# Kernel optimization log

Measured on AMD Instinct MI355X. Metric: run time of the kernel, lower is better.

Reference implementation:

```python
import jax, jax.numpy as jnp
import numpy as np

BITS = 8
BOUND = 2 ** (BITS - 1) - 1  # 127, symmetric int8 as in AQT IntNumerics


def setup_inputs() -> dict:
    key = jax.random.key(0)
    k1, k2 = jax.random.split(key)
    lhs = jax.random.normal(k1, (8192, 4096), dtype=jnp.float32)
    rhs = jax.random.normal(k2, (4096, 4096), dtype=jnp.float32)
    return {"lhs": lhs, "rhs": rhs}


def reference(lhs, rhs):
    # Per-channel symmetric scales over the contracting dim (AQT calibration:
    # abs-max / bound). lhs contracts axis 1, rhs contracts axis 0, per
    # dimension_numbers (((1,),(0,)),((),())).
    lhs_scale = jnp.max(jnp.abs(lhs), axis=1, keepdims=True) / BOUND  # [M,1]
    rhs_scale = jnp.max(jnp.abs(rhs), axis=0, keepdims=True) / BOUND  # [1,N]
    lhs_scale = jnp.where(lhs_scale == 0, jnp.ones_like(lhs_scale), lhs_scale)
    rhs_scale = jnp.where(rhs_scale == 0, jnp.ones_like(rhs_scale), rhs_scale)

    # Quantize: round-to-nearest, clip to [-127, 127], store as int8.
    qlhs = jnp.clip(jnp.round(lhs / lhs_scale), -BOUND, BOUND).astype(jnp.int8)
    qrhs = jnp.clip(jnp.round(rhs / rhs_scale), -BOUND, BOUND).astype(jnp.int8)

    # Integer matmul with int32 accumulation (the AQT quantized dot_general).
    acc = jax.lax.dot_general(
        qlhs, qrhs,
        dimension_numbers=(((1,), (0,)), ((), ())),
        preferred_element_type=jnp.int32,
    )  # [M, N] int32

    # Inline dequant by transposed scales (scale_t): [M,1] * [1,N].
    return acc.astype(jnp.float32) * lhs_scale * rhs_scale
```

## Files before the change

### kernel.cpp

```cpp
#include <hip/hip_runtime.h>
#include <stdint.h>

#define M_DIM 8192
#define N_DIM 4096
#define K_DIM 4096

typedef int v4i __attribute__((ext_vector_type(4)));

typedef __attribute__((address_space(1))) const void gas_void;
typedef __attribute__((address_space(3))) void las_void;

__device__ __forceinline__ void async_copy16(const uint8_t* g, uint8_t* l) {
    __builtin_amdgcn_global_load_lds((gas_void*)g, (las_void*)l, 16, 0, 0);
}

__device__ __forceinline__ int quant1(float x, float scale) {
    float q = __builtin_rintf(x / scale);
    q = fminf(127.0f, fmaxf(-127.0f, q));
    return (int)q;
}

__device__ __forceinline__ uint32_t pack4(int q0, int q1, int q2, int q3) {
    return (uint32_t)(q0 & 255) | ((uint32_t)(q1 & 255) << 8) |
           ((uint32_t)(q2 & 255) << 16) | ((uint32_t)(q3 & 255) << 24);
}

__global__ __launch_bounds__(256) void quant_lhs_kernel(
    const float* __restrict__ lhs, uint8_t* __restrict__ qlhs,
    float* __restrict__ lhs_scale) {
    const int row = blockIdx.x;
    const int tid = threadIdx.x;
    const float4* src = (const float4*)(lhs + (size_t)row * K_DIM);

    float4 v[4];
    float m = 0.0f;
#pragma unroll
    for (int i = 0; i < 4; ++i) {
        v[i] = src[tid + i * 256];
        m = fmaxf(m, fmaxf(fmaxf(fabsf(v[i].x), fabsf(v[i].y)),
                           fmaxf(fabsf(v[i].z), fabsf(v[i].w))));
    }
#pragma unroll
    for (int off = 32; off > 0; off >>= 1)
        m = fmaxf(m, __shfl_down(m, off, 64));

    __shared__ float wmax[4];
    if ((tid & 63) == 0) wmax[tid >> 6] = m;
    __syncthreads();
    const float mm = fmaxf(fmaxf(wmax[0], wmax[1]), fmaxf(wmax[2], wmax[3]));
    const float scale = (mm == 0.0f) ? 1.0f : mm / 127.0f;
    if (tid == 0) lhs_scale[row] = scale;

    uint32_t* dst = (uint32_t*)(qlhs + (size_t)row * K_DIM);
#pragma unroll
    for (int i = 0; i < 4; ++i) {
        dst[tid + i * 256] = pack4(quant1(v[i].x, scale), quant1(v[i].y, scale),
                                   quant1(v[i].z, scale), quant1(v[i].w, scale));
    }
}

__global__ __launch_bounds__(256) void rhs_max_kernel(
    const float* __restrict__ rhs, uint32_t* __restrict__ maxbits) {
    const int c = blockIdx.x * 256 + threadIdx.x;
    const int r0 = blockIdx.y * 128;
    float m = 0.0f;
    for (int r = 0; r < 128; ++r)
        m = fmaxf(m, fabsf(rhs[(size_t)(r0 + r) * N_DIM + c]));
    atomicMax(&maxbits[c], __float_as_uint(m));
}

__global__ __launch_bounds__(256) void rhs_scale_kernel(
    const uint32_t* __restrict__ maxbits, float* __restrict__ rhs_scale) {
    const int c = blockIdx.x * 256 + threadIdx.x;
    const float m = __uint_as_float(maxbits[c]);
    rhs_scale[c] = (m == 0.0f) ? 1.0f : m / 127.0f;
}

__global__ __launch_bounds__(256) void quant_rhs_t_kernel(
    const float* __restrict__ rhs, const float* __restrict__ rhs_scale,
    uint8_t* __restrict__ qrhsT) {
    const int n = blockIdx.x * 256 + threadIdx.x;
    const float scale = rhs_scale[n];
    const int kbase = blockIdx.y * 256;

    for (int c16 = 0; c16 < 16; ++c16) {
        const int k0 = kbase + c16 * 16;
        uint32_t p[4];
#pragma unroll
        for (int g = 0; g < 4; ++g) {
            int q[4];
#pragma unroll
            for (int j = 0; j < 4; ++j) {
                const float x = rhs[(size_t)(k0 + g * 4 + j) * N_DIM + n];
                q[j] = quant1(x, scale);
            }
            p[g] = pack4(q[0], q[1], q[2], q[3]);
        }
        uint4 u;
        u.x = p[0]; u.y = p[1]; u.z = p[2]; u.w = p[3];
        *(uint4*)(qrhsT + (size_t)n * K_DIM + k0) = u;
    }
}

__global__ __launch_bounds__(256) void gemm_i8_kernel(
    const uint8_t* __restrict__ qlhs, const uint8_t* __restrict__ qrhsT,
    const float* __restrict__ lhs_scale, const float* __restrict__ rhs_scale,
    float* __restrict__ out) {
    __shared__ __align__(16) uint8_t As[128 * 64];
    __shared__ __align__(16) uint8_t Bs[128 * 64];

    const int tid = threadIdx.x;
    const int wave = tid >> 6;
    const int lane = tid & 63;

    const int bm = blockIdx.y * 128;
    const int bn = blockIdx.x * 128;

    const int srow = wave * 32 + (lane >> 2);
    const int scol = (lane & 3) * 16;
    const uint8_t* ga = qlhs + (size_t)(bm + srow) * K_DIM + scol;
    const uint8_t* gb = qrhsT + (size_t)(bn + srow) * K_DIM + scol;
    uint8_t* la = As + wave * 2048 + lane * 16;
    uint8_t* lb = Bs + wave * 2048 + lane * 16;
    const size_t rowstep16 = (size_t)16 * K_DIM;

    const int wm = (wave >> 1) * 64;
    const int wn = (wave & 1) * 64;
    const int fra = (wm + (lane & 15)) * 64 + (lane >> 4) * 16;
    const int frb = (wn + (lane & 15)) * 64 + (lane >> 4) * 16;

    v4i acc[4][4] = {};

    for (int k0 = 0; k0 < K_DIM; k0 += 64) {
        async_copy16(ga, la);
        async_copy16(ga + rowstep16, la + 1024);
        async_copy16(gb, lb);
        async_copy16(gb + rowstep16, lb + 1024);
        ga += 64;
        gb += 64;
        __syncthreads();

        v4i a[4], b[4];
#pragma unroll
        for (int i = 0; i < 4; ++i) a[i] = *(const v4i*)(As + fra + i * 1024);
#pragma unroll
        for (int i = 0; i < 4; ++i) b[i] = *(const v4i*)(Bs + frb + i * 1024);
#pragma unroll
        for (int mi = 0; mi < 4; ++mi)
#pragma unroll
            for (int ni = 0; ni < 4; ++ni)
                acc[mi][ni] = __builtin_amdgcn_mfma_i32_16x16x64_i8(
                    a[mi], b[ni], acc[mi][ni], 0, 0, 0);
        __syncthreads();
    }

    const int r0 = bm + wm + (lane >> 4) * 4;
    const int c0 = bn + wn + (lane & 15);
#pragma unroll
    for (int mi = 0; mi < 4; ++mi) {
        float ls[4];
#pragma unroll
        for (int r = 0; r < 4; ++r) ls[r] = lhs_scale[r0 + mi * 16 + r];
#pragma unroll
        for (int ni = 0; ni < 4; ++ni) {
            const int col = c0 + ni * 16;
            const float rs = rhs_scale[col];
            float* o = out + (size_t)(r0 + mi * 16) * N_DIM + col;
#pragma unroll
            for (int r = 0; r < 4; ++r)
                o[(size_t)r * N_DIM] = (float)acc[mi][ni][r] * ls[r] * rs;
        }
    }
}

extern "C" void kernel_launch(void* const* d_in, const int* in_sizes, int n_in,
                              void* d_out, int out_size, void* d_ws,
                              size_t ws_size, hipStream_t stream) {
    const float* lhs = (const float*)d_in[0];
    const float* rhs = (const float*)d_in[1];
    float* out = (float*)d_out;

    uint8_t* ws = (uint8_t*)d_ws;
    uint8_t* qlhs = ws;
    uint8_t* qrhsT = ws + 33554432u;
    float* lhs_scale = (float*)(ws + 50331648u);
    float* rhs_scale = (float*)(ws + 50364416u);
    uint32_t* maxbits = (uint32_t*)(ws + 50380800u);

    hipMemsetAsync(maxbits, 0, N_DIM * sizeof(uint32_t), stream);

    quant_lhs_kernel<<<M_DIM, 256, 0, stream>>>(lhs, qlhs, lhs_scale);
    rhs_max_kernel<<<dim3(N_DIM / 256, 32), 256, 0, stream>>>(rhs, maxbits);
    rhs_scale_kernel<<<N_DIM / 256, 256, 0, stream>>>(maxbits, rhs_scale);
    quant_rhs_t_kernel<<<dim3(N_DIM / 256, K_DIM / 256), 256, 0, stream>>>(
        rhs, rhs_scale, qrhsT);
    gemm_i8_kernel<<<dim3(N_DIM / 128, M_DIM / 128), 256, 0, stream>>>(
        qlhs, qrhsT, lhs_scale, rhs_scale, out);
}
```

Measured before the change: 496.9 us.

## Swizzle GEMM LDS layout, tile rhs quant-transpose through LDS, split rhs max

The int8 GEMM now XOR-swizzles the 16-byte chunk column, both when staging global data into LDS and when reading MFMA fragments, to avoid LDS bank conflicts on the fragment loads. The rhs quantize-transpose kernel is rewritten to read float4 rows coalesced, transpose 64x128 tiles through padded shared memory, and write 16-byte chunks of the transposed int8 output. Previously each thread made strided single-float loads and scattered 16-byte writes. The rhs column-max kernel uses 4x more blocks with shorter unrolled loops for more parallelism, at the cost of more atomics.

```diff
diff --git a/kernel.cpp b/kernel.cpp
--- a/kernel.cpp
+++ b/kernel.cpp
@@ -62,9 +62,10 @@
 __global__ __launch_bounds__(256) void rhs_max_kernel(
     const float* __restrict__ rhs, uint32_t* __restrict__ maxbits) {
     const int c = blockIdx.x * 256 + threadIdx.x;
-    const int r0 = blockIdx.y * 128;
+    const int r0 = blockIdx.y * 32;
     float m = 0.0f;
-    for (int r = 0; r < 128; ++r)
+#pragma unroll
+    for (int r = 0; r < 32; ++r)
         m = fmaxf(m, fabsf(rhs[(size_t)(r0 + r) * N_DIM + c]));
     atomicMax(&maxbits[c], __float_as_uint(m));
 }
@@ -79,26 +80,50 @@
 __global__ __launch_bounds__(256) void quant_rhs_t_kernel(
     const float* __restrict__ rhs, const float* __restrict__ rhs_scale,
     uint8_t* __restrict__ qrhsT) {
-    const int n = blockIdx.x * 256 + threadIdx.x;
-    const float scale = rhs_scale[n];
-    const int kbase = blockIdx.y * 256;
-
-    for (int c16 = 0; c16 < 16; ++c16) {
-        const int k0 = kbase + c16 * 16;
-        uint32_t p[4];
-#pragma unroll
-        for (int g = 0; g < 4; ++g) {
-            int q[4];
-#pragma unroll
-            for (int j = 0; j < 4; ++j) {
-                const float x = rhs[(size_t)(k0 + g * 4 + j) * N_DIM + n];
-                q[j] = quant1(x, scale);
-            }
-            p[g] = pack4(q[0], q[1], q[2], q[3]);
+    __shared__ __align__(16) uint8_t tile[64 * 132];
+    const int nbase = blockIdx.x * 64;
+    const int kbase = blockIdx.y * 128;
+    const int tid = threadIdx.x;
+
+    const int n0 = (tid & 15) * 4;
+    const float s0 = rhs_scale[nbase + n0];
+    const float s1 = rhs_scale[nbase + n0 + 1];
+    const float s2 = rhs_scale[nbase + n0 + 2];
+    const float s3 = rhs_scale[nbase + n0 + 3];
+
+#pragma unroll
+    for (int p = 0; p < 2; ++p) {
+        const int k0 = (tid >> 4) * 4 + p * 64;
+        int q[4][4];
+#pragma unroll
+        for (int i = 0; i < 4; ++i) {
+            const float4 v = *(const float4*)(
+                rhs + (size_t)(kbase + k0 + i) * N_DIM + nbase + n0);
+            q[i][0] = quant1(v.x, s0);
+            q[i][1] = quant1(v.y, s1);
+            q[i][2] = quant1(v.z, s2);
+            q[i][3] = quant1(v.w, s3);
         }
+#pragma unroll
+        for (int j = 0; j < 4; ++j) {
+            *(uint32_t*)(tile + (n0 + j) * 132 + k0) =
+                pack4(q[0][j], q[1][j], q[2][j], q[3][j]);
+        }
+    }
+    __syncthreads();
+
+#pragma unroll
+    for (int p = 0; p < 2; ++p) {
+        const int c = tid + p * 256;
+        const int n = c >> 3;
+        const int g = c & 7;
+        uint32_t d[4];
+#pragma unroll
+        for (int w = 0; w < 4; ++w)
+            d[w] = *(const uint32_t*)(tile + n * 132 + g * 16 + w * 4);
         uint4 u;
-        u.x = p[0]; u.y = p[1]; u.z = p[2]; u.w = p[3];
-        *(uint4*)(qrhsT + (size_t)n * K_DIM + k0) = u;
+        u.x = d[0]; u.y = d[1]; u.z = d[2]; u.w = d[3];
+        *(uint4*)(qrhsT + (size_t)(nbase + n) * K_DIM + kbase + g * 16) = u;
     }
 }
 
@@ -117,7 +142,7 @@
     const int bn = blockIdx.x * 128;
 
     const int srow = wave * 32 + (lane >> 2);
-    const int scol = (lane & 3) * 16;
+    const int scol = ((lane & 3) ^ ((lane >> 3) & 3)) * 16;
     const uint8_t* ga = qlhs + (size_t)(bm + srow) * K_DIM + scol;
     const uint8_t* gb = qrhsT + (size_t)(bn + srow) * K_DIM + scol;
     uint8_t* la = As + wave * 2048 + lane * 16;
@@ -126,8 +151,10 @@
 
     const int wm = (wave >> 1) * 64;
     const int wn = (wave & 1) * 64;
-    const int fra = (wm + (lane & 15)) * 64 + (lane >> 4) * 16;
-    const int frb = (wn + (lane & 15)) * 64 + (lane >> 4) * 16;
+    const int fra =
+        (wm + (lane & 15)) * 64 + (((lane >> 4) ^ ((lane >> 1) & 3)) * 16);
+    const int frb =
+        (wn + (lane & 15)) * 64 + (((lane >> 4) ^ ((lane >> 1) & 3)) * 16);
 
     v4i acc[4][4] = {};
 
@@ -190,9 +217,9 @@
     hipMemsetAsync(maxbits, 0, N_DIM * sizeof(uint32_t), stream);
 
     quant_lhs_kernel<<<M_DIM, 256, 0, stream>>>(lhs, qlhs, lhs_scale);
-    rhs_max_kernel<<<dim3(N_DIM / 256, 32), 256, 0, stream>>>(rhs, maxbits);
+    rhs_max_kernel<<<dim3(N_DIM / 256, 128), 256, 0, stream>>>(rhs, maxbits);
     rhs_scale_kernel<<<N_DIM / 256, 256, 0, stream>>>(maxbits, rhs_scale);
-    quant_rhs_t_kernel<<<dim3(N_DIM / 256, K_DIM / 256), 256, 0, stream>>>(
+    quant_rhs_t_kernel<<<dim3(N_DIM / 64, K_DIM / 128), 256, 0, stream>>>(
         rhs, rhs_scale, qrhsT);
     gemm_i8_kernel<<<dim3(N_DIM / 128, M_DIM / 128), 256, 0, stream>>>(
         qlhs, qrhsT, lhs_scale, rhs_scale, out);
```

After: 440.5 us. -11.4%, faster.
